# Performance work log

Hardware: AMD Instinct MI355X
Metric: run time of the kernel (lower is better)

The kernel has to match this reference:

```python
import jax, jax.numpy as jnp
import numpy as np

B, N, E, ITERS = 8, 1024, 10, 5


def _xavier(key, shape):
    fan_in, fan_out = shape[1], shape[0]
    std = float(np.sqrt(2.0 / (fan_in + fan_out)))
    return jax.random.normal(key, shape, dtype=jnp.float32) * std


def setup_inputs() -> dict:
    key = jax.random.key(0)
    ks = jax.random.split(key, 10)
    return {
        "features": jax.random.uniform(ks[0], (B, N), dtype=jnp.float32),
        "weights": jax.random.uniform(ks[1], (B, N, N), dtype=jnp.float32),
        "adjacency": jax.random.uniform(ks[2], (B, N, N), dtype=jnp.float32),
        # torch Linear(in, out) weight has shape (out, in); y = x @ W.T
        "w_selected": _xavier(ks[3], (E, 1)),
        "w_nbpriors": _xavier(ks[4], (E, E)),
        "w_nbweights": _xavier(ks[5], (E, E)),
        "w_nbweights_ew": _xavier(ks[6], (E, 1)),
        "w_q_reduc": _xavier(ks[7], (1, 2 * E)),
        "w_q_allembed": _xavier(ks[8], (E, E)),
        "w_q_action": _xavier(ks[9], (E, E)),
    }


def reference(features, weights, adjacency, w_selected, w_nbpriors,
              w_nbweights, w_nbweights_ew, w_q_reduc, w_q_allembed, w_q_action):
    b, n = features.shape
    e = w_selected.shape[0]
    # v_selected = Linear(1,E)(features[...,None]) -> outer product with (E,) vector
    v_selected = features[:, :, None] * w_selected[:, 0]            # [B,N,E]
    # relu(Linear(1,E)(weights[...,None])), then sum over dim=1 (source nodes)
    w_exp = jax.nn.relu(weights[:, :, :, None] * w_nbweights_ew[:, 0])  # [B,N,N,E]
    v_weights = jnp.einsum('bje,fe->bjf', jnp.sum(w_exp, axis=1), w_nbweights)  # [B,N,E]
    base = v_selected + v_weights

    embeddings = jnp.zeros((b, n, e), dtype=features.dtype)
    for _ in range(ITERS):
        v_priors = jnp.einsum('bij,bje->bie', adjacency, embeddings)  # [B,N,E]
        v_priors = jnp.einsum('bie,fe->bif', v_priors, w_nbpriors)
        embeddings = jax.nn.relu(base + v_priors)

    sumembed = jnp.einsum('bne,fe->bf', embeddings, w_q_allembed)     # [B,E]
    sumembed = jnp.broadcast_to(sumembed[:, None, :], (b, n, e))
    peract = jnp.einsum('bne,fe->bnf', embeddings, w_q_action)        # [B,N,E]
    q_in = jnp.concatenate([sumembed, peract], axis=2)                # [B,N,2E]
    q_vals = jnp.einsum('bnk,ok->bno', q_in, w_q_reduc)[:, :, 0]      # [B,N]
    return q_vals, embeddings
```

## Files before the change

### kernel.cpp

```cpp
#include <hip/hip_runtime.h>

#define B 8
#define N 1024
#define E 10
#define GP 44
#define EMB_FLOATS (256 * GP)
#define EMB_F4 (EMB_FLOATS / 4)

__global__ __launch_bounds__(512) void k_base(
    const float* __restrict__ W, const float* __restrict__ features,
    const float* __restrict__ w_sel, const float* __restrict__ w_nbw,
    const float* __restrict__ w_ew, float* __restrict__ base,
    float* __restrict__ emb0, float* __restrict__ qsum)
{
    __shared__ float red[2][16][32];
    __shared__ float scol[2][32];
    int bx = blockIdx.x, tid = threadIdx.x;
    int b = bx >> 5, c0 = (bx & 31) * 32;
    int col = tid & 31, rg = tid >> 5;
    const float* wp = W + ((size_t)b * N + rg * 64) * N + c0 + col;
    float sp = 0.f, sn = 0.f;
#pragma unroll 8
    for (int i = 0; i < 64; ++i) {
        float w = wp[(size_t)i * N];
        sp += fmaxf(w, 0.f);
        sn += fmaxf(-w, 0.f);
    }
    red[0][rg][col] = sp;
    red[1][rg][col] = sn;
    __syncthreads();
    if (tid < 64) {
        int which = tid >> 5, cc = tid & 31;
        float t = 0.f;
#pragma unroll
        for (int g = 0; g < 16; ++g) t += red[which][g][cc];
        scol[which][cc] = t;
    }
    __syncthreads();
    if (tid < 32 * E) {
        int cc = tid / E, f = tid % E;
        float spc = scol[0][cc], snc = scol[1][cc];
        float acc = features[(b << 10) + c0 + cc] * w_sel[f];
#pragma unroll
        for (int e = 0; e < E; ++e) {
            float c = w_ew[e];
            float se = (c > 0.f) ? c * spc : (-c) * snc;
            acc += w_nbw[f * E + e] * se;
        }
        int row = c0 + cc;
        base[(size_t)((b << 10) + row) * E + f] = acc;
        emb0[(size_t)b * EMB_FLOATS + (row >> 2) * GP + (row & 3) * E + f] =
            fmaxf(acc, 0.f);
    }
    if (bx == 0 && tid < B) qsum[tid] = 0.f;
}

template <int FINAL>
__global__ __launch_bounds__(256) void k_iter(
    const float* __restrict__ A, const float* __restrict__ ein,
    const float* __restrict__ base, const float* __restrict__ Wp,
    const float* __restrict__ w_reduc, const float* __restrict__ w_all,
    const float* __restrict__ w_act, float* __restrict__ eout,
    float* __restrict__ emb_out, float* __restrict__ qv,
    float* __restrict__ qsum)
{
    __shared__ float4 EmS[EMB_F4];
    __shared__ float vred[4][8][4 * E];
    __shared__ float WpS[E * E];
    __shared__ float gaS[E], gactS[E];
    __shared__ float vS[16 * E], qS[16 * E], qrow[16];

    int bx = blockIdx.x, tid = threadIdx.x;
    int b = bx >> 6, tile = bx & 63;
    int i0 = tile * 16;
    int m = tid >> 6;
    int s = tid & 63;

    float Arf[4][4][4];
    {
        const float* Ab = A + ((size_t)(b * N) + i0 + m) * N + 4 * s;
#pragma unroll
        for (int k = 0; k < 4; ++k)
#pragma unroll
            for (int c = 0; c < 4; ++c) {
                float4 t = *(const float4*)(Ab + (size_t)(4 * k) * N + 256 * c);
                Arf[k][c][0] = t.x; Arf[k][c][1] = t.y;
                Arf[k][c][2] = t.z; Arf[k][c][3] = t.w;
            }
    }

    if (tid < E * E) WpS[tid] = Wp[tid];
    if (FINAL && tid < E) {
        float sa = 0.f, sc = 0.f;
#pragma unroll
        for (int k = 0; k < E; ++k) {
            sa += w_reduc[k] * w_all[k * E + tid];
            sc += w_reduc[E + k] * w_act[k * E + tid];
        }
        gaS[tid] = sa;
        gactS[tid] = sc;
    }

    {
        const float4* src = (const float4*)ein + (size_t)b * EMB_F4;
        float4 tmp[11];
#pragma unroll
        for (int t = 0; t < 11; ++t) tmp[t] = src[tid + 256 * t];
#pragma unroll
        for (int t = 0; t < 11; ++t) EmS[tid + 256 * t] = tmp[t];
    }
    __syncthreads();

    float acc[4][E];
#pragma unroll
    for (int k = 0; k < 4; ++k)
#pragma unroll
        for (int e = 0; e < E; ++e) acc[k][e] = 0.f;

#pragma unroll
    for (int c = 0; c < 4; ++c) {
        float4 g4[10];
        const float4* gp = EmS + (size_t)(s + 64 * c) * (GP / 4);
#pragma unroll
        for (int t = 0; t < 10; ++t) g4[t] = gp[t];
        const float* g40 = (const float*)g4;
#pragma unroll
        for (int q = 0; q < 4; ++q)
#pragma unroll
            for (int k = 0; k < 4; ++k) {
                float a = Arf[k][c][q];
#pragma unroll
                for (int e = 0; e < E; ++e)
                    acc[k][e] += a * g40[q * E + e];
            }
    }

#pragma unroll
    for (int mask = 1; mask <= 4; mask <<= 1)
#pragma unroll
        for (int k = 0; k < 4; ++k)
#pragma unroll
            for (int e = 0; e < E; ++e)
                acc[k][e] += __shfl_xor(acc[k][e], mask, 64);
    if ((s & 7) == 0)
#pragma unroll
        for (int k = 0; k < 4; ++k)
#pragma unroll
            for (int e = 0; e < E; ++e)
                vred[m][s >> 3][k * E + e] = acc[k][e];
    __syncthreads();

    if (tid < 16 * E) {
        int r = tid / E, f = tid % E;
        int mm = r & 3, kk = r >> 2;
        float v[E];
#pragma unroll
        for (int e = 0; e < E; ++e) {
            float t = 0.f;
#pragma unroll
            for (int g = 0; g < 8; ++g) t += vred[mm][g][kk * E + e];
            v[e] = t;
        }
        float d = 0.f;
#pragma unroll
        for (int e = 0; e < E; ++e) d += v[e] * WpS[f * E + e];
        size_t gi = (size_t)((b << 10) + i0 + r);
        float r_out = fmaxf(base[gi * E + f] + d, 0.f);
        if (FINAL) {
            emb_out[gi * E + f] = r_out;
            vS[tid] = r_out * gactS[f];
            qS[tid] = r_out * gaS[f];
        } else {
            int grow = i0 + r;
            eout[(size_t)b * EMB_FLOATS + (grow >> 2) * GP + (grow & 3) * E + f] = r_out;
        }
    }
    if (FINAL) {
        __syncthreads();
        if (tid < 16) {
            float da = 0.f, dg = 0.f;
#pragma unroll
            for (int f = 0; f < E; ++f) {
                da += vS[tid * E + f];
                dg += qS[tid * E + f];
            }
            qv[(b << 10) + i0 + tid] = da;
            qrow[tid] = dg;
        }
        __syncthreads();
        if (tid == 0) {
            float t = 0.f;
#pragma unroll
            for (int r = 0; r < 16; ++r) t += qrow[r];
            atomicAdd(&qsum[b], t);
        }
    }
}

__global__ __launch_bounds__(256) void k_q(float* __restrict__ qv,
                                           const float* __restrict__ qsum) {
    int g = blockIdx.x * 256 + threadIdx.x;
    qv[g] += qsum[g >> 10];
}

extern "C" void kernel_launch(void* const* d_in, const int* in_sizes, int n_in,
                              void* d_out, int out_size, void* d_ws, size_t ws_size,
                              hipStream_t stream) {
    const float* features  = (const float*)d_in[0];
    const float* W         = (const float*)d_in[1];
    const float* adjacency = (const float*)d_in[2];
    const float* w_sel     = (const float*)d_in[3];
    const float* w_pri     = (const float*)d_in[4];
    const float* w_nbw     = (const float*)d_in[5];
    const float* w_ew      = (const float*)d_in[6];
    const float* w_reduc   = (const float*)d_in[7];
    const float* w_all     = (const float*)d_in[8];
    const float* w_act     = (const float*)d_in[9];

    float* out     = (float*)d_out;
    float* qv      = out;
    float* emb_out = out + B * N;

    float* ws   = (float*)d_ws;
    float* eA   = ws;
    float* eB   = eA + (size_t)B * EMB_FLOATS;
    float* base = eB + (size_t)B * EMB_FLOATS;
    float* qsum = base + (size_t)B * N * E;

    k_base<<<256, 512, 0, stream>>>(W, features, w_sel, w_nbw, w_ew,
                                    base, eA, qsum);
    k_iter<0><<<512, 256, 0, stream>>>(adjacency, eA, base, w_pri, w_reduc,
                                       w_all, w_act, eB, emb_out, qv, qsum);
    k_iter<0><<<512, 256, 0, stream>>>(adjacency, eB, base, w_pri, w_reduc,
                                       w_all, w_act, eA, emb_out, qv, qsum);
    k_iter<0><<<512, 256, 0, stream>>>(adjacency, eA, base, w_pri, w_reduc,
                                       w_all, w_act, eB, emb_out, qv, qsum);
    k_iter<1><<<512, 256, 0, stream>>>(adjacency, eB, base, w_pri, w_reduc,
                                       w_all, w_act, nullptr, emb_out, qv, qsum);
    k_q<<<32, 256, 0, stream>>>(qv, qsum);
}
```

Baseline: 157.5 us.

## Vectorize weight column reduction and fuse q broadcast via last-block counter

The base kernel now reads the weight matrix with float4 loads over 16-row groups and reduces 64 partials per column in shared memory, replacing scalar 64-row strided loads. The separate k_q kernel is removed. The final iteration kernel now uses a per-batch atomic counter with threadfence, so the last block of each batch adds the batch-wide q sum to all 1024 q values. This saves one kernel launch. The cost is extra atomics and a serial tail in one block per batch.

```diff
diff --git a/kernel.cpp b/kernel.cpp
--- a/kernel.cpp
+++ b/kernel.cpp
@@ -13,28 +13,33 @@
     const float* __restrict__ w_ew, float* __restrict__ base,
     float* __restrict__ emb0, float* __restrict__ qsum)
 {
-    __shared__ float red[2][16][32];
+    __shared__ float redP[64][32];
+    __shared__ float redN[64][32];
     __shared__ float scol[2][32];
     int bx = blockIdx.x, tid = threadIdx.x;
     int b = bx >> 5, c0 = (bx & 31) * 32;
-    int col = tid & 31, rg = tid >> 5;
-    const float* wp = W + ((size_t)b * N + rg * 64) * N + c0 + col;
-    float sp = 0.f, sn = 0.f;
+    int c4 = (tid & 7) * 4;
+    int rg = tid >> 3;
+    const float* wp = W + ((size_t)b * N + rg * 16) * N + c0 + c4;
+    float4 sp = {0.f, 0.f, 0.f, 0.f}, sn = {0.f, 0.f, 0.f, 0.f};
+#pragma unroll
+    for (int i = 0; i < 16; ++i) {
+        float4 w = *(const float4*)(wp + (size_t)i * N);
+        sp.x += fmaxf(w.x, 0.f); sn.x += fmaxf(-w.x, 0.f);
+        sp.y += fmaxf(w.y, 0.f); sn.y += fmaxf(-w.y, 0.f);
+        sp.z += fmaxf(w.z, 0.f); sn.z += fmaxf(-w.z, 0.f);
+        sp.w += fmaxf(w.w, 0.f); sn.w += fmaxf(-w.w, 0.f);
+    }
+    *(float4*)&redP[rg][c4] = sp;
+    *(float4*)&redN[rg][c4] = sn;
+    __syncthreads();
+    if (tid < 64) {
+        int cc = tid & 31;
+        const float* rp = (tid < 32) ? &redP[0][0] : &redN[0][0];
+        float t = 0.f;
 #pragma unroll 8
-    for (int i = 0; i < 64; ++i) {
-        float w = wp[(size_t)i * N];
-        sp += fmaxf(w, 0.f);
-        sn += fmaxf(-w, 0.f);
-    }
-    red[0][rg][col] = sp;
-    red[1][rg][col] = sn;
-    __syncthreads();
-    if (tid < 64) {
-        int which = tid >> 5, cc = tid & 31;
-        float t = 0.f;
-#pragma unroll
-        for (int g = 0; g < 16; ++g) t += red[which][g][cc];
-        scol[which][cc] = t;
+        for (int g = 0; g < 64; ++g) t += rp[g * 32 + cc];
+        scol[tid >> 5][cc] = t;
     }
     __syncthreads();
     if (tid < 32 * E) {
@@ -52,7 +57,7 @@
         emb0[(size_t)b * EMB_FLOATS + (row >> 2) * GP + (row & 3) * E + f] =
             fmaxf(acc, 0.f);
     }
-    if (bx == 0 && tid < B) qsum[tid] = 0.f;
+    if (bx == 0 && tid < 16) ((float*)qsum)[tid] = 0.f;
 }
 
 template <int FINAL>
@@ -62,13 +67,14 @@
     const float* __restrict__ w_reduc, const float* __restrict__ w_all,
     const float* __restrict__ w_act, float* __restrict__ eout,
     float* __restrict__ emb_out, float* __restrict__ qv,
-    float* __restrict__ qsum)
+    float* __restrict__ qsum, int* __restrict__ counter)
 {
     __shared__ float4 EmS[EMB_F4];
     __shared__ float vred[4][8][4 * E];
     __shared__ float WpS[E * E];
     __shared__ float gaS[E], gactS[E];
     __shared__ float vS[16 * E], qS[16 * E], qrow[16];
+    __shared__ int lastFlag;
 
     int bx = blockIdx.x, tid = threadIdx.x;
     int b = bx >> 6, tile = bx & 63;
@@ -193,14 +199,21 @@
 #pragma unroll
             for (int r = 0; r < 16; ++r) t += qrow[r];
             atomicAdd(&qsum[b], t);
-        }
-    }
-}
-
-__global__ __launch_bounds__(256) void k_q(float* __restrict__ qv,
-                                           const float* __restrict__ qsum) {
-    int g = blockIdx.x * 256 + threadIdx.x;
-    qv[g] += qsum[g >> 10];
+            __threadfence();
+            int old = atomicAdd(&counter[b], 1);
+            lastFlag = (old == 63) ? 1 : 0;
+        }
+        __syncthreads();
+        if (lastFlag) {
+            __threadfence();
+            float S = atomicAdd(&qsum[b], 0.f);
+#pragma unroll
+            for (int k = 0; k < 4; ++k) {
+                int idx = (b << 10) + tid + 256 * k;
+                qv[idx] += S;
+            }
+        }
+    }
 }
 
 extern "C" void kernel_launch(void* const* d_in, const int* in_sizes, int n_in,
@@ -221,21 +234,21 @@
     float* qv      = out;
     float* emb_out = out + B * N;
 
-    float* ws   = (float*)d_ws;
-    float* eA   = ws;
-    float* eB   = eA + (size_t)B * EMB_FLOATS;
-    float* base = eB + (size_t)B * EMB_FLOATS;
-    float* qsum = base + (size_t)B * N * E;
+    float* ws      = (float*)d_ws;
+    float* eA      = ws;
+    float* eB      = eA + (size_t)B * EMB_FLOATS;
+    float* base    = eB + (size_t)B * EMB_FLOATS;
+    float* qsum    = base + (size_t)B * N * E;
+    int*   counter = (int*)(qsum + B);
 
     k_base<<<256, 512, 0, stream>>>(W, features, w_sel, w_nbw, w_ew,
                                     base, eA, qsum);
     k_iter<0><<<512, 256, 0, stream>>>(adjacency, eA, base, w_pri, w_reduc,
-                                       w_all, w_act, eB, emb_out, qv, qsum);
+                                       w_all, w_act, eB, emb_out, qv, qsum, counter);
     k_iter<0><<<512, 256, 0, stream>>>(adjacency, eB, base, w_pri, w_reduc,
-                                       w_all, w_act, eA, emb_out, qv, qsum);
+                                       w_all, w_act, eA, emb_out, qv, qsum, counter);
     k_iter<0><<<512, 256, 0, stream>>>(adjacency, eA, base, w_pri, w_reduc,
-                                       w_all, w_act, eB, emb_out, qv, qsum);
+                                       w_all, w_act, eB, emb_out, qv, qsum, counter);
     k_iter<1><<<512, 256, 0, stream>>>(adjacency, eB, base, w_pri, w_reduc,
-                                       w_all, w_act, nullptr, emb_out, qv, qsum);
-    k_q<<<32, 256, 0, stream>>>(qv, qsum);
+                                       w_all, w_act, eA, emb_out, qv, qsum, counter);
 }
```

After: 163.5 us. +3.8%, slower.
